# Performance work log

Measured on AMD Instinct MI355X. Metric: run time of the kernel, lower is better.

## Reference

```python
import jax, jax.numpy as jnp
import numpy as np

M, K, N, R = 8192, 4096, 4096, 64  # tokens, in_features, out_features, pod_rank


def _unpack_int4(packed):
    """Unpack bytes (stored as int32 in [0,256)) into signed int4 values in [-8,7].
    Low nibble is element 2k, high nibble is element 2k+1."""
    b = packed.astype(jnp.int32)
    low = ((b & 0xF) ^ 8) - 8
    high = (((b >> 4) & 0xF) ^ 8) - 8
    out = jnp.stack([low, high], axis=-1)
    return out.reshape(packed.shape[:-1] + (packed.shape[-1] * 2,))


def setup_inputs() -> dict:
    key = jax.random.key(0)
    ks = jax.random.split(key, 7)
    x_quant = jax.random.randint(ks[0], (M, K // 2), 0, 256, dtype=jnp.int32)
    x_scale = jax.random.uniform(ks[1], (M,), dtype=jnp.float32) * 0.01 + 1e-4
    weight = jax.random.randint(ks[2], (N, K // 2), 0, 256, dtype=jnp.int32)
    weight_scales = jax.random.uniform(ks[3], (N, 1), dtype=jnp.float32) * 0.01 + 1e-4
    bias = jax.random.normal(ks[4], (N,), dtype=jnp.float32) * 0.02
    x_r = jax.random.normal(ks[5], (M, R), dtype=jnp.float32)
    w_outlier = jax.random.normal(ks[6], (N, R), dtype=jnp.float32) * 0.02
    return {"x_quant": x_quant, "x_scale": x_scale, "weight": weight,
            "weight_scales": weight_scales, "bias": bias, "x_r": x_r,
            "w_outlier": w_outlier}


def reference(x_quant, x_scale, weight, weight_scales, bias, x_r, w_outlier):
    xi = _unpack_int4(x_quant)          # [M, K] int32 in [-8,7]
    wi = _unpack_int4(weight)           # [N, K] int32 in [-8,7]
    y_int = jnp.matmul(xi, wi.T)        # [M, N] int32 accumulator
    # dequant: per-token activation scale * per-channel weight scale, plus bias
    y = (y_int.astype(jnp.float32) * x_scale[:, None] * weight_scales.reshape(1, -1)
         + bias[None, :])
    # fused low-rank outlier correction: addmm_(x_r, w_outlier.T)
    y = y + jnp.matmul(x_r, w_outlier.T)
    return y
```

## Files before the change

### kernel.cpp

```cpp
#include <hip/hip_runtime.h>
#include <hip/hip_fp16.h>

typedef int      v4i __attribute__((ext_vector_type(4)));
typedef int      v2i __attribute__((ext_vector_type(2)));
typedef float    v4f __attribute__((ext_vector_type(4)));
typedef _Float16 v8h __attribute__((ext_vector_type(8)));
typedef _Float16 v4h __attribute__((ext_vector_type(4)));

#define MDIM 8192
#define NDIM 4096
#define KDIM 4096
#define RDIM 64
#define KW   (KDIM / 2)
#define NHALF (KDIM / 64)

typedef const __attribute__((address_space(1))) char* gas_ptr;
typedef __attribute__((address_space(3))) char*       las_ptr;

__device__ __forceinline__ void unpack_w(v4i w, int& lo8, int& hi8) {
    unsigned p01 = __builtin_amdgcn_perm((unsigned)w.y, (unsigned)w.x, 0x0C0C0400u);
    unsigned p23 = __builtin_amdgcn_perm((unsigned)w.w, (unsigned)w.z, 0x0C0C0400u);
    unsigned b4  = __builtin_amdgcn_perm(p23, p01, 0x05040100u);
    unsigned lo = b4 & 0x0F0F0F0Fu;
    unsigned hi = (b4 >> 4) & 0x0F0F0F0Fu;
    lo8 = (int)(((lo ^ 0x08080808u) + 0x78787878u) ^ 0x80808080u);
    hi8 = (int)(((hi ^ 0x08080808u) + 0x78787878u) ^ 0x80808080u);
}

__global__ __launch_bounds__(256)
void repack_int4(const int* __restrict__ xq, const int* __restrict__ wq,
                 char* __restrict__ x8, char* __restrict__ w8)
{
    const size_t XCH = (size_t)MDIM * KW / 4;
    const size_t TCH = XCH + (size_t)NDIM * KW / 4;
    size_t stride = (size_t)gridDim.x * blockDim.x;
    for (size_t i = (size_t)blockIdx.x * blockDim.x + threadIdx.x; i < TCH; i += stride) {
        const int* src;
        char* dst;
        if (i < XCH) { src = xq + i * 4; dst = x8 + i * 8; }
        else { size_t j = i - XCH; src = wq + j * 4; dst = w8 + j * 8; }
        v4i w = *(const v4i*)src;
        int lo8, hi8;
        unpack_w(w, lo8, hi8);
        *(v2i*)dst = (v2i){lo8, hi8};
    }
}

__device__ __forceinline__ void stageA(const char* g, char* l, int hh) {
    const char* s = g + hh * 64;
    __builtin_amdgcn_global_load_lds((gas_ptr)(const void*)s,
                                     (las_ptr)(void*)l, 16, 0, 0);
    __builtin_amdgcn_global_load_lds((gas_ptr)(const void*)(s + (size_t)16 * KDIM),
                                     (las_ptr)(void*)(l + 1024), 16, 0, 0);
}
__device__ __forceinline__ void stageB(const char* g, char* l, int hh) {
    __builtin_amdgcn_global_load_lds((gas_ptr)(const void*)(g + hh * 64),
                                     (las_ptr)(void*)l, 16, 0, 0);
}

#define BAR   asm volatile("s_barrier" ::: "memory")
#define VM3   asm volatile("s_waitcnt vmcnt(3)" ::: "memory")
#define LGKM0 do { asm volatile("s_waitcnt lgkmcnt(0)" ::: "memory");          \
                   __builtin_amdgcn_sched_barrier(0); } while (0)

#define READ_A4(dst, BASE)                                                     \
    _Pragma("unroll")                                                          \
    for (int ii = 0; ii < 4; ++ii)                                             \
        dst[ii] = *(const v4i*)((BASE) + aoff + ii * 1024)

#define READ_B4(dst, BASE)                                                     \
    _Pragma("unroll")                                                          \
    for (int jj = 0; jj < 4; ++jj)                                             \
        dst[jj] = *(const v4i*)((BASE) + boff + jj * 1024)

#define MMA16(AS, BS)                                                          \
    __builtin_amdgcn_s_setprio(1);                                             \
    _Pragma("unroll")                                                          \
    for (int ii = 0; ii < 4; ++ii)                                             \
        _Pragma("unroll")                                                      \
        for (int jj = 0; jj < 4; ++jj)                                         \
            acc[ii][jj] = __builtin_amdgcn_mfma_i32_16x16x64_i8(               \
                AS[ii], BS[jj], acc[ii][jj], 0, 0, 0);                         \
    __builtin_amdgcn_s_setprio(0)

__global__ __launch_bounds__(512, 4)
void w4a4_gemm2(const char* __restrict__ x8, const char* __restrict__ w8,
                const float* __restrict__ xsc, const float* __restrict__ wsc,
                const float* __restrict__ bias, const float* __restrict__ xr,
                const float* __restrict__ wo, float* __restrict__ out)
{
    __shared__ __align__(16) char Ahalf[2][16384];
    __shared__ __align__(16) char Bhalf[2][8192];
    __shared__ float xs_s[256];
    __shared__ float ws_s[128];
    __shared__ float bs_s[128];

    const int tid  = threadIdx.x;
    const int lane = tid & 63;
    const int wid  = tid >> 6;
    const int wm   = wid >> 1;
    const int wn   = wid & 1;

    const int s  = (blockIdx.x & 7) * 128 + (blockIdx.x >> 3);
    const int by = s >> 5;
    const int bxn = s & 31;

    if (tid < 256) {
        xs_s[tid] = xsc[by * 256 + tid];
    } else if (tid < 384) {
        int n = tid - 256;
        ws_s[n] = wsc[bxn * 128 + n];
        bs_s[n] = bias[bxn * 128 + n];
    }

    const int scol  = ((lane & 3) * 16) ^ (((lane >> 3) & 3) << 4);
    const int srowA = wid * 32 + (lane >> 2);
    const int srowB = wid * 16 + (lane >> 2);
    const char* gA = x8 + (size_t)(by * 256 + srowA) * KDIM + scol;
    const char* gB = w8 + (size_t)(bxn * 128 + srowB) * KDIM + scol;
    const int ldsWA = wid * 2048;
    const int ldsWB = wid * 1024;

    const int lr   = lane & 15;
    const int cef  = ((lane >> 4) << 4) ^ (((lr >> 1) & 3) << 4);
    const int aoff = (wm * 64 + lr) * 64 + cef;
    const int boff = (wn * 64 + lr) * 64 + cef;

    v4i acc[4][4];
#pragma unroll
    for (int i = 0; i < 4; ++i)
#pragma unroll
        for (int j = 0; j < 4; ++j) acc[i][j] = (v4i){0, 0, 0, 0};

    stageA(gA, &Ahalf[0][ldsWA], 0);
    stageB(gB, &Bhalf[0][ldsWB], 0);
    stageA(gA, &Ahalf[1][ldsWA], 1);
    stageB(gB, &Bhalf[1][ldsWB], 1);
    VM3;
    BAR;

    v4i fa[4], fb[4];
    for (int h = 0; h < NHALF; ++h) {
        const char* Ab = &Ahalf[h & 1][0];
        const char* Bb = &Bhalf[h & 1][0];
        READ_A4(fa, Ab);
        READ_B4(fb, Bb);
        LGKM0;
        BAR;
        int hn = h + 2;
        if (hn > NHALF - 1) hn = NHALF - 1;
        stageA(gA, &Ahalf[h & 1][ldsWA], hn);
        stageB(gB, &Bhalf[h & 1][ldsWB], hn);
        __builtin_amdgcn_sched_barrier(0);
        MMA16(fa, fb);
        VM3;
        BAR;
    }

    asm volatile("s_waitcnt vmcnt(0)" ::: "memory");
    BAR;

    char* Xh = (char*)&Ahalf[0][0];
    char* Wh = (char*)&Bhalf[0][0];
    {
        const int rr = tid >> 3;
        const int cb = (tid & 7) * 16;
#pragma unroll
        for (int p = 0; p < 4; ++p) {
            const int row = p * 64 + rr;
            const int sw = cb ^ ((row & 7) << 4);
            v4f x0 = *(const v4f*)(xr + (size_t)(by * 256 + row) * RDIM + (cb >> 1));
            v4f x1 = *(const v4f*)(xr + (size_t)(by * 256 + row) * RDIM + (cb >> 1) + 4);
            v8h hx = {(_Float16)x0[0], (_Float16)x0[1], (_Float16)x0[2], (_Float16)x0[3],
                      (_Float16)x1[0], (_Float16)x1[1], (_Float16)x1[2], (_Float16)x1[3]};
            *(v8h*)(Xh + (size_t)row * 128 + sw) = hx;
            if (p < 2) {
                v4f w0 = *(const v4f*)(wo + (size_t)(bxn * 128 + row) * RDIM + (cb >> 1));
                v4f w1 = *(const v4f*)(wo + (size_t)(bxn * 128 + row) * RDIM + (cb >> 1) + 4);
                v8h hw = {(_Float16)w0[0], (_Float16)w0[1], (_Float16)w0[2], (_Float16)w0[3],
                          (_Float16)w1[0], (_Float16)w1[1], (_Float16)w1[2], (_Float16)w1[3]};
                *(v8h*)(Wh + (size_t)row * 128 + sw) = hw;
            }
        }
    }

#pragma unroll
    for (int i = 0; i < 4; ++i) {
        const int r0 = wm * 64 + i * 16 + ((lane >> 4) << 2);
        const v4f xs4 = *(const v4f*)&xs_s[r0];
#pragma unroll
        for (int j = 0; j < 4; ++j) {
            const int col = wn * 64 + j * 16 + lr;
            const float sw = ws_s[col];
            const float bz = bs_s[col];
            v4f f;
#pragma unroll
            for (int r = 0; r < 4; ++r)
                f[r] = (float)acc[i][j][r] * xs4[r] * sw + bz;
            acc[i][j] = __builtin_bit_cast(v4i, f);
        }
    }
    __syncthreads();

#pragma unroll
    for (int ks = 0; ks < 2; ++ks) {
        v8h ah[4], bh[4];
#pragma unroll
        for (int i = 0; i < 4; ++i) {
            const int row = wm * 64 + i * 16 + lr;
            const int c   = (ks * 64 + ((lane >> 4) << 4)) ^ ((row & 7) << 4);
            ah[i] = *(const v8h*)(Xh + (size_t)row * 128 + c);
        }
#pragma unroll
        for (int j = 0; j < 4; ++j) {
            const int row = wn * 64 + j * 16 + lr;
            const int c   = (ks * 64 + ((lane >> 4) << 4)) ^ ((row & 7) << 4);
            bh[j] = *(const v8h*)(Wh + (size_t)row * 128 + c);
        }
#pragma unroll
        for (int i = 0; i < 4; ++i)
#pragma unroll
            for (int j = 0; j < 4; ++j) {
                v4f c = __builtin_bit_cast(v4f, acc[i][j]);
                c = __builtin_amdgcn_mfma_f32_16x16x32_f16(ah[i], bh[j], c, 0, 0, 0);
                acc[i][j] = __builtin_bit_cast(v4i, c);
            }
    }

    const size_t obase = (size_t)(by * 256 + wm * 64 + ((lane >> 4) << 2)) * NDIM
                       + bxn * 128 + wn * 64 + lr;
#pragma unroll
    for (int i = 0; i < 4; ++i)
#pragma unroll
        for (int j = 0; j < 4; ++j) {
            v4f f = __builtin_bit_cast(v4f, acc[i][j]);
#pragma unroll
            for (int r = 0; r < 4; ++r)
                out[obase + (size_t)(i * 16 + r) * NDIM + j * 16] = f[r];
        }
}

__global__ __launch_bounds__(256, 2)
void w4a4_fused(const int* __restrict__ xq, const float* __restrict__ xsc,
                const int* __restrict__ wq, const float* __restrict__ wsc,
                const float* __restrict__ bias, const float* __restrict__ xr,
                const float* __restrict__ wo, float* __restrict__ out)
{
    __shared__ __align__(16) char As[128 * 144];
    __shared__ __align__(16) char Bs[128 * 144];
    __shared__ float xs_s[128];
    __shared__ float ws_s[128];
    __shared__ float bs_s[128];

    const int tid  = threadIdx.x;
    const int lane = tid & 63;
    const int wid  = tid >> 6;
    const int wm   = wid >> 1;
    const int wn   = wid & 1;
    const int bx   = blockIdx.x % (NDIM / 128);
    const int by   = blockIdx.x / (NDIM / 128);

    const int srow   = tid >> 4;
    const int schunk = tid & 15;

    if (tid < 128) {
        xs_s[tid] = xsc[by * 128 + tid];
    } else {
        int n = tid - 128;
        ws_s[n] = wsc[bx * 128 + n];
        bs_s[n] = bias[bx * 128 + n];
    }

    const int* gA = xq + (size_t)(by * 128 + srow) * KW + schunk * 4;
    const int* gB = wq + (size_t)(bx * 128 + srow) * KW + schunk * 4;
    char* lA = As + srow * 144 + schunk * 8;
    char* lB = Bs + srow * 144 + schunk * 8;

    v4i acc[4][4];
#pragma unroll
    for (int i = 0; i < 4; ++i)
#pragma unroll
        for (int j = 0; j < 4; ++j) acc[i][j] = (v4i){0, 0, 0, 0};

    const int lr = lane & 15;
    const int lkb = (lane >> 4) * 16;

    for (int kt = 0; kt < KDIM / 128; ++kt) {
#pragma unroll
        for (int p = 0; p < 8; ++p) {
            v4i w = *(const v4i*)(gA + (size_t)p * 16 * KW + kt * 64);
            int lo8, hi8;
            unpack_w(w, lo8, hi8);
            *(v2i*)(lA + p * 16 * 144) = (v2i){lo8, hi8};
        }
#pragma unroll
        for (int p = 0; p < 8; ++p) {
            v4i w = *(const v4i*)(gB + (size_t)p * 16 * KW + kt * 64);
            int lo8, hi8;
            unpack_w(w, lo8, hi8);
            *(v2i*)(lB + p * 16 * 144) = (v2i){lo8, hi8};
        }
        __syncthreads();
#pragma unroll
        for (int ks = 0; ks < 2; ++ks) {
            v4i av[4], bv[4];
#pragma unroll
            for (int i = 0; i < 4; ++i)
                av[i] = *(const v4i*)(As + (wm * 64 + i * 16 + lr) * 144 + ks * 64 + lkb);
#pragma unroll
            for (int j = 0; j < 4; ++j)
                bv[j] = *(const v4i*)(Bs + (wn * 64 + j * 16 + lr) * 144 + ks * 64 + lkb);
#pragma unroll
            for (int i = 0; i < 4; ++i)
#pragma unroll
                for (int j = 0; j < 4; ++j)
                    acc[i][j] = __builtin_amdgcn_mfma_i32_16x16x64_i8(av[i], bv[j], acc[i][j], 0, 0, 0);
        }
        __syncthreads();
    }

    _Float16* Xh = (_Float16*)As;
    _Float16* Wh = (_Float16*)Bs;
#pragma unroll
    for (int p = 0; p < 8; ++p) {
        int row = p * 16 + srow;
        float4 vx = *(const float4*)(xr + (size_t)(by * 128 + row) * RDIM + schunk * 4);
        *(v4h*)(Xh + row * 72 + schunk * 4) =
            (v4h){(_Float16)vx.x, (_Float16)vx.y, (_Float16)vx.z, (_Float16)vx.w};
        float4 vw = *(const float4*)(wo + (size_t)(bx * 128 + row) * RDIM + schunk * 4);
        *(v4h*)(Wh + row * 72 + schunk * 4) =
            (v4h){(_Float16)vw.x, (_Float16)vw.y, (_Float16)vw.z, (_Float16)vw.w};
    }
    __syncthreads();

    v4f facc[4][4];
#pragma unroll
    for (int i = 0; i < 4; ++i)
#pragma unroll
        for (int j = 0; j < 4; ++j) facc[i][j] = (v4f){0.f, 0.f, 0.f, 0.f};

    const int lkh = (lane >> 4) * 8;
#pragma unroll
    for (int ks = 0; ks < 2; ++ks) {
        v8h ah[4], bh[4];
#pragma unroll
        for (int i = 0; i < 4; ++i)
            ah[i] = *(const v8h*)(Xh + (wm * 64 + i * 16 + lr) * 72 + ks * 32 + lkh);
#pragma unroll
        for (int j = 0; j < 4; ++j)
            bh[j] = *(const v8h*)(Wh + (wn * 64 + j * 16 + lr) * 72 + ks * 32 + lkh);
#pragma unroll
        for (int i = 0; i < 4; ++i)
#pragma unroll
            for (int j = 0; j < 4; ++j)
                facc[i][j] = __builtin_amdgcn_mfma_f32_16x16x32_f16(ah[i], bh[j], facc[i][j], 0, 0, 0);
    }

#pragma unroll
    for (int i = 0; i < 4; ++i) {
        int row0 = wm * 64 + i * 16 + (lane >> 4) * 4;
#pragma unroll
        for (int j = 0; j < 4; ++j) {
            int col = wn * 64 + j * 16 + lr;
            float sw = ws_s[col];
            float bz = bs_s[col];
#pragma unroll
            for (int r = 0; r < 4; ++r) {
                int row = row0 + r;
                float v = (float)acc[i][j][r] * xs_s[row] * sw + bz + facc[i][j][r];
                out[(size_t)(by * 128 + row) * NDIM + (bx * 128 + col)] = v;
            }
        }
    }
}

extern "C" void kernel_launch(void* const* d_in, const int* in_sizes, int n_in,
                              void* d_out, int out_size, void* d_ws, size_t ws_size,
                              hipStream_t stream) {
    const int*   xq   = (const int*)d_in[0];
    const float* xsc  = (const float*)d_in[1];
    const int*   wq   = (const int*)d_in[2];
    const float* wsc  = (const float*)d_in[3];
    const float* bias = (const float*)d_in[4];
    const float* xr   = (const float*)d_in[5];
    const float* wo   = (const float*)d_in[6];
    float* out = (float*)d_out;

    const size_t X8 = (size_t)MDIM * KDIM;
    const size_t W8 = (size_t)NDIM * KDIM;

    if (ws_size >= X8 + W8) {
        char* x8 = (char*)d_ws;
        char* w8 = x8 + X8;
        repack_int4<<<2048, 256, 0, stream>>>(xq, wq, x8, w8);
        w4a4_gemm2<<<(MDIM / 256) * (NDIM / 128), 512, 0, stream>>>(
            x8, w8, xsc, wsc, bias, xr, wo, out);
    } else {
        w4a4_fused<<<(MDIM / 128) * (NDIM / 128), 256, 0, stream>>>(
            xq, xsc, wq, wsc, bias, xr, wo, out);
    }
}
```

Before: 182.3 us.

## Load pre-tiled weight fragments directly to registers, stage only activations in LDS

```diff
diff --git a/kernel.cpp b/kernel.cpp
--- a/kernel.cpp
+++ b/kernel.cpp
@@ -12,7 +12,7 @@
 #define KDIM 4096
 #define RDIM 64
 #define KW   (KDIM / 2)
-#define NHALF (KDIM / 64)
+#define NT   (KDIM / 64)
 
 typedef const __attribute__((address_space(1))) char* gas_ptr;
 typedef __attribute__((address_space(3))) char*       las_ptr;
@@ -29,49 +29,52 @@
 
 __global__ __launch_bounds__(256)
 void repack_int4(const int* __restrict__ xq, const int* __restrict__ wq,
-                 char* __restrict__ x8, char* __restrict__ w8)
+                 char* __restrict__ x8, char* __restrict__ w8t)
 {
     const size_t XCH = (size_t)MDIM * KW / 4;
     const size_t TCH = XCH + (size_t)NDIM * KW / 4;
     size_t stride = (size_t)gridDim.x * blockDim.x;
     for (size_t i = (size_t)blockIdx.x * blockDim.x + threadIdx.x; i < TCH; i += stride) {
-        const int* src;
+        v4i w;
         char* dst;
-        if (i < XCH) { src = xq + i * 4; dst = x8 + i * 8; }
-        else { size_t j = i - XCH; src = wq + j * 4; dst = w8 + j * 8; }
-        v4i w = *(const v4i*)src;
+        if (i < XCH) {
+            w = *(const v4i*)(xq + i * 4);
+            dst = x8 + i * 8;
+        } else {
+            size_t j = i - XCH;
+            w = *(const v4i*)(wq + j * 4);
+            int n  = (int)(j >> 9);
+            int kc = (int)(j & 511);
+            size_t off = (size_t)(n >> 4) * 65536 + (size_t)(kc >> 1) * 256
+                       + (n & 15) * 16 + (kc & 1) * 8;
+            dst = w8t + off;
+        }
         int lo8, hi8;
         unpack_w(w, lo8, hi8);
         *(v2i*)dst = (v2i){lo8, hi8};
     }
 }
 
-__device__ __forceinline__ void stageA(const char* g, char* l, int hh) {
-    const char* s = g + hh * 64;
+__device__ __forceinline__ void stageA(const char* g, char* l, int kt) {
+    const char* s = g + kt * 64;
     __builtin_amdgcn_global_load_lds((gas_ptr)(const void*)s,
                                      (las_ptr)(void*)l, 16, 0, 0);
     __builtin_amdgcn_global_load_lds((gas_ptr)(const void*)(s + (size_t)16 * KDIM),
                                      (las_ptr)(void*)(l + 1024), 16, 0, 0);
 }
-__device__ __forceinline__ void stageB(const char* g, char* l, int hh) {
-    __builtin_amdgcn_global_load_lds((gas_ptr)(const void*)(g + hh * 64),
-                                     (las_ptr)(void*)l, 16, 0, 0);
-}
-
-#define BAR   asm volatile("s_barrier" ::: "memory")
-#define VM3   asm volatile("s_waitcnt vmcnt(3)" ::: "memory")
-#define LGKM0 do { asm volatile("s_waitcnt lgkmcnt(0)" ::: "memory");          \
-                   __builtin_amdgcn_sched_barrier(0); } while (0)
+
+#define BAR asm volatile("s_barrier" ::: "memory")
+#define VM2 asm volatile("s_waitcnt vmcnt(2)" ::: "memory")
 
 #define READ_A4(dst, BASE)                                                     \
     _Pragma("unroll")                                                          \
     for (int ii = 0; ii < 4; ++ii)                                             \
         dst[ii] = *(const v4i*)((BASE) + aoff + ii * 1024)
 
-#define READ_B4(dst, BASE)                                                     \
+#define LOADB(dst, KT)                                                         \
     _Pragma("unroll")                                                          \
     for (int jj = 0; jj < 4; ++jj)                                             \
-        dst[jj] = *(const v4i*)((BASE) + boff + jj * 1024)
+        dst[jj] = *(const v4i*)(gBbase + (size_t)(KT) * 1024 + jj * 65536)
 
 #define MMA16(AS, BS)                                                          \
     __builtin_amdgcn_s_setprio(1);                                             \
@@ -83,15 +86,25 @@
                 AS[ii], BS[jj], acc[ii][jj], 0, 0, 0);                         \
     __builtin_amdgcn_s_setprio(0)
 
-__global__ __launch_bounds__(512, 4)
-void w4a4_gemm2(const char* __restrict__ x8, const char* __restrict__ w8,
+#define PHASE(KT, BU, BF) do {                                                 \
+    const int kt_ = (KT);                                                      \
+    READ_A4(fa, &Asl[kt_ & 3][0]);                                             \
+    const int ktb = (kt_ + 1 < NT) ? kt_ + 1 : NT - 1;                         \
+    LOADB(BF, ktb);                                                            \
+    const int kta = (kt_ + 2 < NT) ? kt_ + 2 : NT - 1;                         \
+    stageA(gA, &Asl[(kt_ + 2) & 3][ldsW], kta);                                \
+    MMA16(fa, BU);                                                             \
+    VM2; BAR;                                                                  \
+} while (0)
+
+__global__ __launch_bounds__(256, 3)
+void w4a4_split(const char* __restrict__ x8, const char* __restrict__ w8t,
                 const float* __restrict__ xsc, const float* __restrict__ wsc,
                 const float* __restrict__ bias, const float* __restrict__ xr,
                 const float* __restrict__ wo, float* __restrict__ out)
 {
-    __shared__ __align__(16) char Ahalf[2][16384];
-    __shared__ __align__(16) char Bhalf[2][8192];
-    __shared__ float xs_s[256];
+    __shared__ __align__(16) char Asl[4][8192];
+    __shared__ float xs_s[128];
     __shared__ float ws_s[128];
     __shared__ float bs_s[128];
 
@@ -101,30 +114,30 @@
     const int wm   = wid >> 1;
     const int wn   = wid & 1;
 
-    const int s  = (blockIdx.x & 7) * 128 + (blockIdx.x >> 3);
-    const int by = s >> 5;
-    const int bxn = s & 31;
-
-    if (tid < 256) {
-        xs_s[tid] = xsc[by * 256 + tid];
-    } else if (tid < 384) {
-        int n = tid - 256;
+    const int xcd = blockIdx.x & 7;
+    const int idx = blockIdx.x >> 3;
+    const int bxn = xcd * 4 + (idx >> 6);
+    const int by  = idx & 63;
+
+    if (tid < 128) {
+        xs_s[tid] = xsc[by * 128 + tid];
+    } else {
+        int n = tid - 128;
         ws_s[n] = wsc[bxn * 128 + n];
         bs_s[n] = bias[bxn * 128 + n];
     }
 
-    const int scol  = ((lane & 3) * 16) ^ (((lane >> 3) & 3) << 4);
-    const int srowA = wid * 32 + (lane >> 2);
-    const int srowB = wid * 16 + (lane >> 2);
-    const char* gA = x8 + (size_t)(by * 256 + srowA) * KDIM + scol;
-    const char* gB = w8 + (size_t)(bxn * 128 + srowB) * KDIM + scol;
-    const int ldsWA = wid * 2048;
-    const int ldsWB = wid * 1024;
-
-    const int lr   = lane & 15;
+    const int scol = ((lane & 3) * 16) ^ (((lane >> 3) & 3) << 4);
+    const int srow = wid * 32 + (lane >> 2);
+    const char* gA = x8 + (size_t)(by * 128 + srow) * KDIM + scol;
+    const int ldsW = wid * 2048;
+
+    const int lr = lane & 15;
+    const char* gBbase = w8t + (size_t)(bxn * 8 + wn * 4) * 65536
+                       + lr * 16 + (lane >> 4) * 256;
+
     const int cef  = ((lane >> 4) << 4) ^ (((lr >> 1) & 3) << 4);
     const int aoff = (wm * 64 + lr) * 64 + cef;
-    const int boff = (wn * 64 + lr) * 64 + cef;
 
     v4i acc[4][4];
 #pragma unroll
@@ -132,55 +145,40 @@
 #pragma unroll
         for (int j = 0; j < 4; ++j) acc[i][j] = (v4i){0, 0, 0, 0};
 
-    stageA(gA, &Ahalf[0][ldsWA], 0);
-    stageB(gB, &Bhalf[0][ldsWB], 0);
-    stageA(gA, &Ahalf[1][ldsWA], 1);
-    stageB(gB, &Bhalf[1][ldsWB], 1);
-    VM3;
-    BAR;
-
-    v4i fa[4], fb[4];
-    for (int h = 0; h < NHALF; ++h) {
-        const char* Ab = &Ahalf[h & 1][0];
-        const char* Bb = &Bhalf[h & 1][0];
-        READ_A4(fa, Ab);
-        READ_B4(fb, Bb);
-        LGKM0;
-        BAR;
-        int hn = h + 2;
-        if (hn > NHALF - 1) hn = NHALF - 1;
-        stageA(gA, &Ahalf[h & 1][ldsWA], hn);
-        stageB(gB, &Bhalf[h & 1][ldsWB], hn);
-        __builtin_amdgcn_sched_barrier(0);
-        MMA16(fa, fb);
-        VM3;
-        BAR;
+    v4i fa[4], bA[4], bB[4];
+
+    stageA(gA, &Asl[0][ldsW], 0);
+    LOADB(bA, 0);
+    stageA(gA, &Asl[1][ldsW], 1);
+    VM2; BAR;
+
+    for (int kt = 0; kt < NT; kt += 2) {
+        PHASE(kt,     bA, bB);
+        PHASE(kt + 1, bB, bA);
     }
 
     asm volatile("s_waitcnt vmcnt(0)" ::: "memory");
     BAR;
 
-    char* Xh = (char*)&Ahalf[0][0];
-    char* Wh = (char*)&Bhalf[0][0];
+    char* Xh = (char*)&Asl[0][0];
+    char* Wh = (char*)&Asl[2][0];
     {
         const int rr = tid >> 3;
         const int cb = (tid & 7) * 16;
 #pragma unroll
         for (int p = 0; p < 4; ++p) {
-            const int row = p * 64 + rr;
+            const int row = p * 32 + rr;
             const int sw = cb ^ ((row & 7) << 4);
-            v4f x0 = *(const v4f*)(xr + (size_t)(by * 256 + row) * RDIM + (cb >> 1));
-            v4f x1 = *(const v4f*)(xr + (size_t)(by * 256 + row) * RDIM + (cb >> 1) + 4);
+            v4f x0 = *(const v4f*)(xr + (size_t)(by * 128 + row) * RDIM + (cb >> 1));
+            v4f x1 = *(const v4f*)(xr + (size_t)(by * 128 + row) * RDIM + (cb >> 1) + 4);
             v8h hx = {(_Float16)x0[0], (_Float16)x0[1], (_Float16)x0[2], (_Float16)x0[3],
                       (_Float16)x1[0], (_Float16)x1[1], (_Float16)x1[2], (_Float16)x1[3]};
             *(v8h*)(Xh + (size_t)row * 128 + sw) = hx;
-            if (p < 2) {
-                v4f w0 = *(const v4f*)(wo + (size_t)(bxn * 128 + row) * RDIM + (cb >> 1));
-                v4f w1 = *(const v4f*)(wo + (size_t)(bxn * 128 + row) * RDIM + (cb >> 1) + 4);
-                v8h hw = {(_Float16)w0[0], (_Float16)w0[1], (_Float16)w0[2], (_Float16)w0[3],
-                          (_Float16)w1[0], (_Float16)w1[1], (_Float16)w1[2], (_Float16)w1[3]};
-                *(v8h*)(Wh + (size_t)row * 128 + sw) = hw;
-            }
+            v4f w0 = *(const v4f*)(wo + (size_t)(bxn * 128 + row) * RDIM + (cb >> 1));
+            v4f w1 = *(const v4f*)(wo + (size_t)(bxn * 128 + row) * RDIM + (cb >> 1) + 4);
+            v8h hw = {(_Float16)w0[0], (_Float16)w0[1], (_Float16)w0[2], (_Float16)w0[3],
+                      (_Float16)w1[0], (_Float16)w1[1], (_Float16)w1[2], (_Float16)w1[3]};
+            *(v8h*)(Wh + (size_t)row * 128 + sw) = hw;
         }
     }
 
@@ -227,7 +225,7 @@
             }
     }
 
-    const size_t obase = (size_t)(by * 256 + wm * 64 + ((lane >> 4) << 2)) * NDIM
+    const size_t obase = (size_t)(by * 128 + wm * 64 + ((lane >> 4) << 2)) * NDIM
                        + bxn * 128 + wn * 64 + lr;
 #pragma unroll
     for (int i = 0; i < 4; ++i)
@@ -390,11 +388,11 @@
     const size_t W8 = (size_t)NDIM * KDIM;
 
     if (ws_size >= X8 + W8) {
-        char* x8 = (char*)d_ws;
-        char* w8 = x8 + X8;
-        repack_int4<<<2048, 256, 0, stream>>>(xq, wq, x8, w8);
-        w4a4_gemm2<<<(MDIM / 256) * (NDIM / 128), 512, 0, stream>>>(
-            x8, w8, xsc, wsc, bias, xr, wo, out);
+        char* x8  = (char*)d_ws;
+        char* w8t = x8 + X8;
+        repack_int4<<<2048, 256, 0, stream>>>(xq, wq, x8, w8t);
+        w4a4_split<<<(MDIM / 128) * (NDIM / 128), 256, 0, stream>>>(
+            x8, w8t, xsc, wsc, bias, xr, wo, out);
     } else {
         w4a4_fused<<<(MDIM / 128) * (NDIM / 128), 256, 0, stream>>>(
             xq, xsc, wq, wsc, bias, xr, wo, out);
```

Result: slower. 217.4 us (+19.3%).
